# Optimization experiments

Measured on AMD Instinct MI355X. Metric: run time of the kernel, lower is better.

## Reference

```python
import jax, jax.numpy as jnp
import numpy as np

B, L, D_IN, H, LATENT, SEG = 8, 4096, 1024, 1024, 256, 128
K = L // SEG  # subsequences per row


def setup_inputs() -> dict:
    key = jax.random.key(0)
    ks = jax.random.split(key, 8)
    sc = 1.0 / np.sqrt(H)
    # periodic segment-end bitmask: 1 at the last position of each length-SEG segment
    mask = jnp.zeros((B, L), jnp.int32).at[:, jnp.arange(SEG - 1, L, SEG)].set(1)
    return {
        "decoder_output": jax.random.normal(ks[0], (B, L, D_IN), jnp.float32),
        "targets": jax.random.normal(ks[1], (B, L, D_IN), jnp.float32),
        "W_proj": jax.random.normal(ks[2], (D_IN, H), jnp.float32) * (1.0 / np.sqrt(D_IN)),
        "b_proj": jnp.zeros((H,), jnp.float32),
        "a_raw": jax.random.normal(ks[3], (H,), jnp.float32),  # decay logits, a = sigmoid(a_raw)
        "W_out": jax.random.normal(ks[4], (H, H), jnp.float32) * sc,
        "b_out": jnp.zeros((H,), jnp.float32),
        "W_mu": jax.random.normal(ks[5], (H, LATENT), jnp.float32) * sc,
        "b_mu": jnp.zeros((LATENT,), jnp.float32),
        "W_lv": jax.random.normal(ks[6], (H, LATENT), jnp.float32) * sc,
        "b_lv": jnp.zeros((LATENT,), jnp.float32),
        "segmentation_indices": mask,
        "num_subseq": K,
    }


def _segment_bounds(mask, L, num_subseq):
    # mask: (B, L) int; positions of ones are inclusive segment ends
    pos = jnp.where(mask.astype(bool), jnp.arange(L)[None, :], L)
    end_incl = jnp.sort(pos, axis=1)[:, :num_subseq]            # (B, K)
    ends = end_incl + 1                                          # exclusive ends
    starts = jnp.concatenate(
        [jnp.zeros((mask.shape[0], 1), ends.dtype), ends[:, :-1]], axis=1)
    return starts, ends


def reference(decoder_output, targets, W_proj, b_proj, a_raw, W_out, b_out,
              W_mu, b_mu, W_lv, b_lv, segmentation_indices, num_subseq):
    Bb, Ll, _ = targets.shape
    starts, ends = _segment_bounds(segmentation_indices, Ll, num_subseq)

    # Step 1: project both streams to hidden (continuous input_proj path)
    u_corr = targets @ W_proj + b_proj          # (B, L, H) correct-context inputs
    u_dec = decoder_output @ W_proj + b_proj    # (B, L, H) decoder inputs
    a = jax.nn.sigmoid(a_raw)                   # (H,) diagonal SSM decay

    t_idx = jnp.arange(Ll)

    # Steps 2-5: for subsequence k, the mixer sequence is correct embeddings on
    # [0, start_k) (the prefix context) followed by decoder embeddings on
    # [start_k, end_k); we take the hidden state at end_k - 1 (carry frozen after).
    def run_one(uc, ud, s, e):
        def step(h, inp):
            t, uct, udt = inp
            u = jnp.where(t < s, uct, udt)
            h_new = a * h + u
            return jnp.where(t < e, h_new, h), None
        h0 = jnp.zeros_like(uc[0])
        hT, _ = jax.lax.scan(step, h0, (t_idx, uc, ud))
        return hT

    run_k = jax.vmap(run_one, in_axes=(None, None, 0, 0))   # over K subsequences
    run_bk = jax.vmap(run_k, in_axes=(0, 0, 0, 0))          # over batch
    hT = run_bk(u_corr, u_dec, starts, ends)                # (B, K, H)

    # Step 6: heads on last hidden state
    y = jax.nn.silu(hT @ W_out + b_out)                     # mixer output proj
    mu_q = y @ W_mu + b_mu                                  # (B, K, LATENT)
    logvar_q = y @ W_lv + b_lv                              # (B, K, LATENT)
    return mu_q, logvar_q
```

## Files before the change

kernel.cpp:

```cpp
#include <hip/hip_runtime.h>
#include <hip/hip_bf16.h>
#include <cstdint>
#include <cstddef>

#define B_DIM 8
#define L_DIM 4096
#define D_INN 1024
#define H_DIM 1024
#define LATENTD 256
#define SEGLEN 128
#define KSUB 32
#define M_HALF (B_DIM * L_DIM)
#define M_TOTAL (2 * M_HALF)

typedef __attribute__((ext_vector_type(8))) short bf16x8;
typedef __attribute__((ext_vector_type(4))) float f32x4;

static __device__ __forceinline__ unsigned short f2bf(float x) {
  __hip_bfloat16 b = __float2bfloat16(x);
  return __builtin_bit_cast(unsigned short, b);
}

static __device__ __forceinline__ void async16(const unsigned short* g, unsigned short* l) {
  __builtin_amdgcn_global_load_lds(
      (const __attribute__((address_space(1))) unsigned int*)g,
      (__attribute__((address_space(3))) unsigned int*)l,
      16, 0, 0);
}


__global__ __launch_bounds__(256) void decay_kernel(const float* __restrict__ a_raw,
                                                    float* __restrict__ avec,
                                                    float* __restrict__ gvec,
                                                    float* __restrict__ a128v) {
  int h = blockIdx.x * 256 + threadIdx.x;
  if (h >= H_DIM) return;
  float a = 1.f / (1.f + expf(-a_raw[h]));
  float p = 1.f, g = 0.f;
  for (int j = 0; j < SEGLEN; j++) { g += p; p *= a; }
  avec[h] = a; gvec[h] = g; a128v[h] = p;
}

__global__ __launch_bounds__(256) void wproj_transpose_kernel(const float* __restrict__ W,
                                                              unsigned short* __restrict__ WT) {
  __shared__ float tile[64][65];
  int d0 = blockIdx.x * 64, h0 = blockIdx.y * 64;
  for (int i = threadIdx.x; i < 64 * 64; i += 256) {
    int dd = i >> 6, hh = i & 63;
    tile[dd][hh] = W[(size_t)(d0 + dd) * H_DIM + h0 + hh];
  }
  __syncthreads();
  for (int i = threadIdx.x; i < 64 * 64; i += 256) {
    int hh = i >> 6, dd = i & 63;
    WT[(size_t)(h0 + hh) * D_INN + d0 + dd] = f2bf(tile[dd][hh]);
  }
}

__global__ __launch_bounds__(256) void prep2_kernel(const float* __restrict__ Wo,
                                                    const float* __restrict__ Wm,
                                                    const float* __restrict__ Wl,
                                                    unsigned short* __restrict__ WoutT,
                                                    unsigned short* __restrict__ WcatT) {
  __shared__ float tile[64][65];
  int z = blockIdx.z;
  const float* src; unsigned short* dst; int N; int rowoff;
  if (z == 0)      { src = Wo; dst = WoutT; N = 1024; rowoff = 0; }
  else if (z == 1) { src = Wm; dst = WcatT; N = 256;  rowoff = 0; }
  else             { src = Wl; dst = WcatT; N = 256;  rowoff = 256; }
  int k0 = blockIdx.x * 64, n0 = blockIdx.y * 64;
  if (n0 >= N) return;
  for (int i = threadIdx.x; i < 64 * 64; i += 256) {
    int kk = i >> 6, nn = i & 63;
    tile[kk][nn] = src[(size_t)(k0 + kk) * N + n0 + nn];
  }
  __syncthreads();
  for (int i = threadIdx.x; i < 64 * 64; i += 256) {
    int nn = i >> 6, kk = i & 63;
    dst[(size_t)(rowoff + n0 + nn) * 1024 + k0 + kk] = f2bf(tile[kk][nn]);
  }
}


__global__ __launch_bounds__(512) void gemm_seg_kernel(const float* __restrict__ Atgt,
                                                       const float* __restrict__ Adec,
                                                       const unsigned short* __restrict__ WT,
                                                       const float* __restrict__ avec,
                                                       const float* __restrict__ gvec,
                                                       const float* __restrict__ bproj,
                                                       float* __restrict__ Dred) {
  __shared__ alignas(16) unsigned short lds[65536];

  const int t = threadIdx.x;
  const int lane = t & 63;
  const int wave = t >> 6;
  const int wr = wave >> 2;
  const int wc = wave & 3;
  const int lo = lane & 15;
  const int q = lane >> 4;

  const int bid = blockIdx.x;
  const int w = (bid & 7) * 128 + (bid >> 3);
  const int bn = w & 3;
  const int bm = w >> 2;

  const int tr = t >> 3;
  const int csw = (((t & 7) ^ (tr & 7)) * 8);
  const unsigned short* Bsrc = WT + ((size_t)(bn * 256 + tr)) * 1024 + csw;
  unsigned short* ldsB = lds + 32768 + t * 8;

#define STAGEB(buf_, tile_)                                                        \
  {                                                                                \
    _Pragma("unroll")                                                              \
    for (int hl = 0; hl < 4; ++hl) {                                               \
      const int half_ = hl >> 1, l_ = hl & 1;                                      \
      async16(Bsrc + (size_t)(half_ * 128 + l_ * 64) * 1024 + (tile_) * 64,        \
              ldsB + (buf_) * 16384 + half_ * 8192 + l_ * 4096);                   \
    }                                                                              \
  }

  const float* Afp = ((bm < 128) ? Atgt : Adec) + ((size_t)(bm & 127)) * 256 * 1024;
  const float* Ath = Afp + ((size_t)(t >> 4)) * 1024 + (t & 15) * 4;
  const int awr_swz = (((((t & 15) >> 1)) ^ ((t >> 4) & 7)) * 8) + (t & 1) * 4;
  unsigned short* ldsAw = lds + ((t >> 4) * 64) + awr_swz;

  float4 fA[8];

#define ALOAD(tile_)                                                               \
  {                                                                                \
    _Pragma("unroll")                                                              \
    for (int i_ = 0; i_ < 8; ++i_)                                                 \
      fA[i_] = *(const float4*)(Ath + (size_t)i_ * 32768 + (tile_) * 64);          \
  }

#define AWRITE(buf_)                                                               \
  {                                                                                \
    _Pragma("unroll")                                                              \
    for (int i_ = 0; i_ < 8; ++i_) {                                               \
      ushort4 o_;                                                                  \
      o_.x = f2bf(fA[i_].x); o_.y = f2bf(fA[i_].y);                                \
      o_.z = f2bf(fA[i_].z); o_.w = f2bf(fA[i_].w);                                \
      *(ushort4*)(ldsAw + (buf_) * 16384 + i_ * 2048) = o_;                        \
    }                                                                              \
  }

  const unsigned short* ArdB = lds + (size_t)(wr * 128 + lo) * 64;
  const unsigned short* BrdB = lds + 32768 + (size_t)(wc * 64 + lo) * 64;
  const int ch0 = ((q ^ (lo & 7)) * 8);
  const int ch1 = (((4 + q) ^ (lo & 7)) * 8);

  f32x4 acc[8][4];
#pragma unroll
  for (int i = 0; i < 8; i++)
#pragma unroll
    for (int j = 0; j < 4; j++) acc[i][j] = (f32x4){0.f, 0.f, 0.f, 0.f};

  ALOAD(0);
  __builtin_amdgcn_sched_barrier(0);
  STAGEB(0, 0);
  __builtin_amdgcn_sched_barrier(0);
  AWRITE(0);
  ALOAD(1);
  __builtin_amdgcn_sched_barrier(0);
  STAGEB(1, 1);
  __builtin_amdgcn_sched_barrier(0);
  AWRITE(1);
  asm volatile("s_waitcnt lgkmcnt(0)" ::: "memory");
  __builtin_amdgcn_sched_barrier(0);

  int buf = 0;
  for (int tile = 0; tile < 16; ++tile) {
    if (tile == 15) asm volatile("s_waitcnt vmcnt(0)" ::: "memory");
    asm volatile("s_barrier" ::: "memory");
    __builtin_amdgcn_sched_barrier(0);

    const unsigned short* Ab = ArdB + buf * 16384;
    const unsigned short* Bb = BrdB + buf * 16384;

    bf16x8 a0[8], b0[4];
#pragma unroll
    for (int i = 0; i < 8; i++) a0[i] = *(const bf16x8*)&Ab[i * 1024 + ch0];
#pragma unroll
    for (int j = 0; j < 4; j++) b0[j] = *(const bf16x8*)&Bb[j * 1024 + ch0];
#pragma unroll
    for (int i = 0; i < 8; i++)
#pragma unroll
      for (int j = 0; j < 4; j++)
        acc[i][j] = __builtin_amdgcn_mfma_f32_16x16x32_bf16(a0[i], b0[j], acc[i][j], 0, 0, 0);

    bf16x8 a1[8], b1[4];
#pragma unroll
    for (int i = 0; i < 8; i++) a1[i] = *(const bf16x8*)&Ab[i * 1024 + ch1];
#pragma unroll
    for (int j = 0; j < 4; j++) b1[j] = *(const bf16x8*)&Bb[j * 1024 + ch1];

    asm volatile("s_waitcnt lgkmcnt(0)" ::: "memory");
    __builtin_amdgcn_sched_barrier(0);
    asm volatile("s_barrier" ::: "memory");

    if (tile < 14) {
      ALOAD(tile + 2);
      __builtin_amdgcn_sched_barrier(0);
      STAGEB(buf, tile + 2);
    }

    __builtin_amdgcn_s_setprio(1);
#pragma unroll
    for (int i = 0; i < 8; i++)
#pragma unroll
      for (int j = 0; j < 4; j++)
        acc[i][j] = __builtin_amdgcn_mfma_f32_16x16x32_bf16(a1[i], b1[j], acc[i][j], 0, 0, 0);
    __builtin_amdgcn_s_setprio(0);
    __builtin_amdgcn_sched_barrier(0);

    if (tile < 14) {
      asm volatile("s_waitcnt vmcnt(4)" ::: "memory");
      __builtin_amdgcn_sched_barrier(0);
      AWRITE(buf);
    }
    buf ^= 1;
  }
#undef STAGEB
#undef ALOAD
#undef AWRITE

  const int seg = bm * 2 + wr;
#pragma unroll
  for (int j = 0; j < 4; ++j) {
    const int h = bn * 256 + wc * 64 + j * 16 + lo;
    const float a = avec[h];
    const float a2 = a * a, a4 = a2 * a2, a8 = a4 * a4, a16 = a8 * a8;
    float P = 0.f;
#pragma unroll
    for (int i = 0; i < 8; ++i) {
      f32x4 u = acc[i][j];
      float vi = ((u.x * a + u.y) * a + u.z) * a + u.w;
      P = P * a16 + vi;
    }
    const float qf = (q == 3) ? 1.f : ((q == 2) ? a4 : ((q == 1) ? a8 : a8 * a4));
    P *= qf;
    P += __shfl_xor(P, 16);
    P += __shfl_xor(P, 32);
    if (q == 0)
      Dred[(size_t)seg * H_DIM + h] = P + bproj[h] * gvec[h];
  }
}

__global__ __launch_bounds__(256) void state_kernel(const float* __restrict__ Dred,
                                                    const float* __restrict__ a128v,
                                                    unsigned short* __restrict__ hTbf) {
  int idx = blockIdx.x * 256 + threadIdx.x;
  int b = idx >> 10, h = idx & 1023;
  const float* S = Dred + (size_t)b * KSUB * H_DIM + h;
  const float* Dd = Dred + (size_t)(B_DIM + b) * KSUB * H_DIM + h;
  float A = a128v[h];
  float C = 0.f;
  for (int k = 0; k < KSUB; k++) {
    hTbf[((size_t)(b * KSUB + k)) * H_DIM + h] = f2bf(fmaf(A, C, Dd[(size_t)k * H_DIM]));
    C = fmaf(A, C, S[(size_t)k * H_DIM]);
  }
}

__global__ __launch_bounds__(256) void head1_kernel(const unsigned short* __restrict__ Abf,
                                                    const unsigned short* __restrict__ Bt,
                                                    const float* __restrict__ bias,
                                                    unsigned short* __restrict__ ybf) {
  __shared__ alignas(16) unsigned short As[128 * 32];
  __shared__ alignas(16) unsigned short Bs[128 * 32];
  const int t = threadIdx.x;
  const int lane = t & 63, wave = t >> 6;
  const int bm = blockIdx.x, bn = blockIdx.y;
  const int lo = lane & 15, q = lane >> 4;
  const int wm = wave & 1, wn = wave >> 1;

  f32x4 acc[4][4];
#pragma unroll
  for (int i = 0; i < 4; i++)
#pragma unroll
    for (int j = 0; j < 4; j++) acc[i][j] = (f32x4){0.f, 0.f, 0.f, 0.f};

  const int r0 = t >> 2;
  const int c0 = (t & 3) * 8;
  const unsigned short* Ag0 = Abf + ((size_t)bm * 128 + r0) * 1024 + c0;
  const unsigned short* Ag1 = Abf + ((size_t)bm * 128 + 64 + r0) * 1024 + c0;
  const unsigned short* Bg0 = Bt + ((size_t)bn * 128 + r0) * 1024 + c0;
  const unsigned short* Bg1 = Bt + ((size_t)bn * 128 + 64 + r0) * 1024 + c0;
  unsigned short* Al0 = &As[t * 8];
  unsigned short* Al1 = &As[(256 + t) * 8];
  unsigned short* Bl0 = &Bs[t * 8];
  unsigned short* Bl1 = &Bs[(256 + t) * 8];

  for (int kk = 0; kk < 1024; kk += 32) {
    async16(Ag0 + kk, Al0);
    async16(Ag1 + kk, Al1);
    async16(Bg0 + kk, Bl0);
    async16(Bg1 + kk, Bl1);
    __syncthreads();
    bf16x8 af[4], bv[4];
#pragma unroll
    for (int i = 0; i < 4; i++)
      af[i] = *(const bf16x8*)&As[(wm * 64 + i * 16 + lo) * 32 + q * 8];
#pragma unroll
    for (int j = 0; j < 4; j++)
      bv[j] = *(const bf16x8*)&Bs[(wn * 64 + j * 16 + lo) * 32 + q * 8];
#pragma unroll
    for (int i = 0; i < 4; i++)
#pragma unroll
      for (int j = 0; j < 4; j++)
        acc[i][j] = __builtin_amdgcn_mfma_f32_16x16x32_bf16(af[i], bv[j], acc[i][j], 0, 0, 0);
    __syncthreads();
  }

#pragma unroll
  for (int j = 0; j < 4; j++) {
    const int col = bn * 128 + wn * 64 + j * 16 + lo;
    const float bb = bias[col];
#pragma unroll
    for (int i = 0; i < 4; i++) {
#pragma unroll
      for (int r = 0; r < 4; r++) {
        const int row = bm * 128 + wm * 64 + i * 16 + q * 4 + r;
        float z = acc[i][j][r] + bb;
        float y = z / (1.f + expf(-z));
        ybf[(size_t)row * 1024 + col] = f2bf(y);
      }
    }
  }
}

__global__ __launch_bounds__(256) void head2_kernel(const unsigned short* __restrict__ Abf,
                                                    const unsigned short* __restrict__ Bt,
                                                    const float* __restrict__ bmu,
                                                    const float* __restrict__ blv,
                                                    float* __restrict__ out) {
  __shared__ alignas(16) unsigned short As[128 * 32];
  __shared__ alignas(16) unsigned short Bs[128 * 32];
  const int t = threadIdx.x;
  const int lane = t & 63, wave = t >> 6;
  const int bm = blockIdx.x, bn = blockIdx.y;
  const int lo = lane & 15, q = lane >> 4;
  const int wm = wave & 1, wn = wave >> 1;

  f32x4 acc[4][4];
#pragma unroll
  for (int i = 0; i < 4; i++)
#pragma unroll
    for (int j = 0; j < 4; j++) acc[i][j] = (f32x4){0.f, 0.f, 0.f, 0.f};

  const int r0 = t >> 2;
  const int c0 = (t & 3) * 8;
  const unsigned short* Ag0 = Abf + ((size_t)bm * 128 + r0) * 1024 + c0;
  const unsigned short* Ag1 = Abf + ((size_t)bm * 128 + 64 + r0) * 1024 + c0;
  const unsigned short* Bg0 = Bt + ((size_t)bn * 128 + r0) * 1024 + c0;
  const unsigned short* Bg1 = Bt + ((size_t)bn * 128 + 64 + r0) * 1024 + c0;
  unsigned short* Al0 = &As[t * 8];
  unsigned short* Al1 = &As[(256 + t) * 8];
  unsigned short* Bl0 = &Bs[t * 8];
  unsigned short* Bl1 = &Bs[(256 + t) * 8];

  for (int kk = 0; kk < 1024; kk += 32) {
    async16(Ag0 + kk, Al0);
    async16(Ag1 + kk, Al1);
    async16(Bg0 + kk, Bl0);
    async16(Bg1 + kk, Bl1);
    __syncthreads();
    bf16x8 af[4], bv[4];
#pragma unroll
    for (int i = 0; i < 4; i++)
      af[i] = *(const bf16x8*)&As[(wm * 64 + i * 16 + lo) * 32 + q * 8];
#pragma unroll
    for (int j = 0; j < 4; j++)
      bv[j] = *(const bf16x8*)&Bs[(wn * 64 + j * 16 + lo) * 32 + q * 8];
#pragma unroll
    for (int i = 0; i < 4; i++)
#pragma unroll
      for (int j = 0; j < 4; j++)
        acc[i][j] = __builtin_amdgcn_mfma_f32_16x16x32_bf16(af[i], bv[j], acc[i][j], 0, 0, 0);
    __syncthreads();
  }

#pragma unroll
  for (int j = 0; j < 4; j++) {
    const int col = bn * 128 + wn * 64 + j * 16 + lo;
    const float bb = (col < 256) ? bmu[col] : blv[col - 256];
    float* dst = (col < 256) ? (out + col) : (out + 65536 + (col - 256));
#pragma unroll
    for (int i = 0; i < 4; i++) {
#pragma unroll
      for (int r = 0; r < 4; r++) {
        const int row = bm * 128 + wm * 64 + i * 16 + q * 4 + r;
        dst[(size_t)row * 256] = acc[i][j][r] + bb;
      }
    }
  }
}

extern "C" void kernel_launch(void* const* d_in, const int* in_sizes, int n_in,
                              void* d_out, int out_size, void* d_ws, size_t ws_size,
                              hipStream_t stream) {
  const float* decoder = (const float*)d_in[0];
  const float* targets = (const float*)d_in[1];
  const float* W_proj = (const float*)d_in[2];
  const float* b_proj = (const float*)d_in[3];
  const float* a_raw = (const float*)d_in[4];
  const float* W_out = (const float*)d_in[5];
  const float* b_out = (const float*)d_in[6];
  const float* W_mu = (const float*)d_in[7];
  const float* b_mu = (const float*)d_in[8];
  const float* W_lv = (const float*)d_in[9];
  const float* b_lv = (const float*)d_in[10];
  float* out = (float*)d_out;

  char* ws = (char*)d_ws;
  unsigned short* WT = (unsigned short*)(ws + 134217728);
  float* avec = (float*)(ws + 136314880);
  float* gvec = (float*)(ws + 136318976);
  float* a128v = (float*)(ws + 136323072);
  float* DredP = (float*)(ws + 136327168);
  unsigned short* hTbf = (unsigned short*)ws;
  unsigned short* ybf = (unsigned short*)(ws + 524288);
  unsigned short* WoutT = (unsigned short*)(ws + 1048576);
  unsigned short* WcatT = (unsigned short*)(ws + 3145728);

  decay_kernel<<<4, 256, 0, stream>>>(a_raw, avec, gvec, a128v);
  wproj_transpose_kernel<<<dim3(16, 16), 256, 0, stream>>>(W_proj, WT);
  gemm_seg_kernel<<<1024, 512, 0, stream>>>(targets, decoder, WT, avec, gvec, b_proj, DredP);
  prep2_kernel<<<dim3(16, 16, 3), 256, 0, stream>>>(W_out, W_mu, W_lv, WoutT, WcatT);
  state_kernel<<<32, 256, 0, stream>>>(DredP, a128v, hTbf);
  head1_kernel<<<dim3(2, 8), 256, 0, stream>>>(hTbf, WoutT, b_out, ybf);
  head2_kernel<<<dim3(2, 4), 256, 0, stream>>>(ybf, WcatT, b_mu, b_lv, out);
}
```

Measured before the change: 475.5 us.

## Merge prep kernels into one launch and deepen A-tile prefetch pipeline

Folds the decay, W_proj transpose and head-weight transpose kernels into one prep_kernel launch, which removes two kernel launches. In the main GEMM the fp32 A-tile register loads now run one tile further ahead: A for tile+3 is issued right after writing tile+1 to LDS, while B staging stays two tiles ahead. This is meant to hide global-load latency of the fp32 activations behind more MFMA work. In exchange it keeps more registers live, and the vmcnt wait counts must still line up with the new load order.

```diff
diff --git a/kernel.cpp b/kernel.cpp
--- a/kernel.cpp
+++ b/kernel.cpp
@@ -28,45 +28,33 @@
       16, 0, 0);
 }
 
-
-__global__ __launch_bounds__(256) void decay_kernel(const float* __restrict__ a_raw,
-                                                    float* __restrict__ avec,
-                                                    float* __restrict__ gvec,
-                                                    float* __restrict__ a128v) {
-  int h = blockIdx.x * 256 + threadIdx.x;
-  if (h >= H_DIM) return;
-  float a = 1.f / (1.f + expf(-a_raw[h]));
-  float p = 1.f, g = 0.f;
-  for (int j = 0; j < SEGLEN; j++) { g += p; p *= a; }
-  avec[h] = a; gvec[h] = g; a128v[h] = p;
-}
-
-__global__ __launch_bounds__(256) void wproj_transpose_kernel(const float* __restrict__ W,
-                                                              unsigned short* __restrict__ WT) {
+__global__ __launch_bounds__(256) void prep_kernel(const float* __restrict__ W_proj,
+                                                   const float* __restrict__ a_raw,
+                                                   const float* __restrict__ Wo,
+                                                   const float* __restrict__ Wm,
+                                                   const float* __restrict__ Wl,
+                                                   unsigned short* __restrict__ WT,
+                                                   float* __restrict__ avec,
+                                                   float* __restrict__ gvec,
+                                                   float* __restrict__ a128v,
+                                                   unsigned short* __restrict__ WoutT,
+                                                   unsigned short* __restrict__ WcatT) {
+  const int z = blockIdx.z;
+  if (z == 4) {
+    if (blockIdx.y != 0 || blockIdx.x >= 4) return;
+    int h = blockIdx.x * 256 + threadIdx.x;
+    float a = 1.f / (1.f + expf(-a_raw[h]));
+    float p = 1.f, g = 0.f;
+    for (int j = 0; j < SEGLEN; j++) { g += p; p *= a; }
+    avec[h] = a; gvec[h] = g; a128v[h] = p;
+    return;
+  }
   __shared__ float tile[64][65];
-  int d0 = blockIdx.x * 64, h0 = blockIdx.y * 64;
-  for (int i = threadIdx.x; i < 64 * 64; i += 256) {
-    int dd = i >> 6, hh = i & 63;
-    tile[dd][hh] = W[(size_t)(d0 + dd) * H_DIM + h0 + hh];
-  }
-  __syncthreads();
-  for (int i = threadIdx.x; i < 64 * 64; i += 256) {
-    int hh = i >> 6, dd = i & 63;
-    WT[(size_t)(h0 + hh) * D_INN + d0 + dd] = f2bf(tile[dd][hh]);
-  }
-}
-
-__global__ __launch_bounds__(256) void prep2_kernel(const float* __restrict__ Wo,
-                                                    const float* __restrict__ Wm,
-                                                    const float* __restrict__ Wl,
-                                                    unsigned short* __restrict__ WoutT,
-                                                    unsigned short* __restrict__ WcatT) {
-  __shared__ float tile[64][65];
-  int z = blockIdx.z;
   const float* src; unsigned short* dst; int N; int rowoff;
-  if (z == 0)      { src = Wo; dst = WoutT; N = 1024; rowoff = 0; }
-  else if (z == 1) { src = Wm; dst = WcatT; N = 256;  rowoff = 0; }
-  else             { src = Wl; dst = WcatT; N = 256;  rowoff = 256; }
+  if (z == 0)      { src = W_proj; dst = WT;    N = 1024; rowoff = 0; }
+  else if (z == 1) { src = Wo;     dst = WoutT; N = 1024; rowoff = 0; }
+  else if (z == 2) { src = Wm;     dst = WcatT; N = 256;  rowoff = 0; }
+  else             { src = Wl;     dst = WcatT; N = 256;  rowoff = 256; }
   int k0 = blockIdx.x * 64, n0 = blockIdx.y * 64;
   if (n0 >= N) return;
   for (int i = threadIdx.x; i < 64 * 64; i += 256) {
@@ -157,13 +145,16 @@
   ALOAD(0);
   __builtin_amdgcn_sched_barrier(0);
   STAGEB(0, 0);
+  STAGEB(1, 1);
   __builtin_amdgcn_sched_barrier(0);
+  asm volatile("s_waitcnt vmcnt(8)" ::: "memory");
   AWRITE(0);
   ALOAD(1);
   __builtin_amdgcn_sched_barrier(0);
-  STAGEB(1, 1);
+  asm volatile("s_waitcnt vmcnt(0)" ::: "memory");
+  AWRITE(1);
+  ALOAD(2);
   __builtin_amdgcn_sched_barrier(0);
-  AWRITE(1);
   asm volatile("s_waitcnt lgkmcnt(0)" ::: "memory");
   __builtin_amdgcn_sched_barrier(0);
 
@@ -197,11 +188,7 @@
     __builtin_amdgcn_sched_barrier(0);
     asm volatile("s_barrier" ::: "memory");
 
-    if (tile < 14) {
-      ALOAD(tile + 2);
-      __builtin_amdgcn_sched_barrier(0);
-      STAGEB(buf, tile + 2);
-    }
+    if (tile < 14) STAGEB(buf, tile + 2);
 
     __builtin_amdgcn_s_setprio(1);
 #pragma unroll
@@ -216,6 +203,8 @@
       asm volatile("s_waitcnt vmcnt(4)" ::: "memory");
       __builtin_amdgcn_sched_barrier(0);
       AWRITE(buf);
+      if (tile < 13) ALOAD(tile + 3);
+      __builtin_amdgcn_sched_barrier(0);
     }
     buf ^= 1;
   }
@@ -421,10 +410,9 @@
   unsigned short* WoutT = (unsigned short*)(ws + 1048576);
   unsigned short* WcatT = (unsigned short*)(ws + 3145728);
 
-  decay_kernel<<<4, 256, 0, stream>>>(a_raw, avec, gvec, a128v);
-  wproj_transpose_kernel<<<dim3(16, 16), 256, 0, stream>>>(W_proj, WT);
+  prep_kernel<<<dim3(16, 16, 5), 256, 0, stream>>>(W_proj, a_raw, W_out, W_mu, W_lv,
+                                                   WT, avec, gvec, a128v, WoutT, WcatT);
   gemm_seg_kernel<<<1024, 512, 0, stream>>>(targets, decoder, WT, avec, gvec, b_proj, DredP);
-  prep2_kernel<<<dim3(16, 16, 3), 256, 0, stream>>>(W_out, W_mu, W_lv, WoutT, WcatT);
   state_kernel<<<32, 256, 0, stream>>>(DredP, a128v, hTbf);
   head1_kernel<<<dim3(2, 8), 256, 0, stream>>>(hTbf, WoutT, b_out, ybf);
   head2_kernel<<<dim3(2, 4), 256, 0, stream>>>(ybf, WcatT, b_mu, b_lv, out);
```

After: 434.4 us. -8.6%, faster.
